# Kernel tuning notes

Measured on AMD Instinct MI355X. Metric: run time of the kernel, lower is better.

Reference implementation:

```python
import jax, jax.numpy as jnp
import numpy as np

B, N, K = 4, 8192, 10
_DIMS = [(12, 64), (64, 64), (128, 64), (64, 64), (128, 64), (192, 1024), (1216, 256), (256, 256), (256, 128), (128, 2)]


def setup_inputs() -> dict:
    key = jax.random.key(0)
    keys = jax.random.split(key, 12)
    inp = {"targets": jax.random.normal(keys[0], (B, N, 3), dtype=jnp.float32)}
    for i, (ci, co) in enumerate(_DIMS):
        a = float(np.sqrt(0.75 / ci))  # init_params: uniform(-sqrt(0.75/fan_in), +)
        inp[f"w{i + 1}"] = jax.random.uniform(keys[i + 1], (ci, co), minval=-a, maxval=a, dtype=jnp.float32)
    inp["prelu_a"] = 0.25 * jnp.ones((10,), jnp.float32)  # nn.PReLU default slope
    return inp


def _prelu(x, a):
    return jnp.where(x >= 0, x, a * x)


def _graph_features(x, k):
    # x: [N, C] -> edge features [N, k, 2C] (knn gather, diff, concat center)
    x2 = jnp.sum(x * x, axis=-1)
    d = x2[:, None] + x2[None, :] - 2.0 * (x @ x.T)  # [N, N] sq dists
    _, idx = jax.lax.top_k(-d, k)  # k nearest (includes self)
    nb = x[idx]  # [N, k, C]
    xr = jnp.broadcast_to(x[:, None, :], nb.shape)
    return jnp.concatenate([nb - xr, xr], axis=-1)


def _edge_conv(x, wa_list, k):
    # x: [B, N, C]; shared-MLP on edge features then max over k neighbors
    f = jax.vmap(lambda xb: _graph_features(xb, k))(x)  # [B, N, k, 2C]
    for w, a in wa_list:
        f = _prelu(f @ w, a)
    return jnp.max(f, axis=-2)  # [B, N, Cout]


def _forward(targets, ws, pa):
    # loss_f(targets) = 0.5*||targets||^2  =>  targets_grad = targets
    g = jax.grad(lambda t: 0.5 * jnp.sum(t * t))(targets)
    x = jnp.concatenate([targets, g], axis=-1)  # [B, N, 6]; hidden_features=0
    x1 = _edge_conv(x, [(ws[0], pa[0]), (ws[1], pa[1])], K)
    x2 = _edge_conv(x1, [(ws[2], pa[2]), (ws[3], pa[3])], K)
    x3 = _edge_conv(x2, [(ws[4], pa[4])], K)
    x4 = jnp.concatenate([x1, x2, x3], axis=-1)  # [B, N, 192]
    x5 = _prelu(x4 @ ws[5], pa[5])  # [B, N, 1024]
    x5 = jnp.broadcast_to(jnp.max(x5, axis=-2, keepdims=True), x5.shape)  # global max, repeated
    y = jnp.concatenate([x1, x2, x3, x5], axis=-1)  # [B, N, 1216]
    for i in range(6, 10):  # dropout is identity at eval
        y = _prelu(y @ ws[i], pa[i])
    return y[..., : 2]  # lr = y[..., :num_losses*2]; hidden slice is empty


def reference(targets, w1, w2, w3, w4, w5, w6, w7, w8, w9, w10, prelu_a):
    ws = [w1, w2, w3, w4, w5, w6, w7, w8, w9, w10]
    return _forward(targets, ws, prelu_a)
```

## Files before the change

kernel.cpp:

```cpp
#include <hip/hip_runtime.h>
#include <math.h>

#define NPTS 8192
#define KNNK 10

typedef __attribute__((ext_vector_type(8))) short bf16x8s;
typedef __attribute__((ext_vector_type(4))) float f32x4;

__device__ __forceinline__ float preluf(float v, float a){ return v >= 0.f ? v : a*v; }
__device__ __forceinline__ float4 f4fma(float a, float4 b, float4 c){
  return make_float4(fmaf(a,b.x,c.x), fmaf(a,b.y,c.y), fmaf(a,b.z,c.z), fmaf(a,b.w,c.w));
}

__device__ __forceinline__ void gl_lds16(const void* g, void* l){
  __builtin_amdgcn_global_load_lds((const __attribute__((address_space(1))) void*)g,
                                   (__attribute__((address_space(3))) void*)l, 16, 0, 0);
}
__device__ __forceinline__ void gl_lds4(const void* g, void* l){
  __builtin_amdgcn_global_load_lds((const __attribute__((address_space(1))) void*)g,
                                   (__attribute__((address_space(3))) void*)l, 4, 0, 0);
}

__device__ __forceinline__ void kinsd2(double* bk, float& g9, float pbd9, float d, int j){
  if (__any(d < g9)) {
    double t = (double)d;
    t = __longlong_as_double(__double_as_longlong(t) | (unsigned long long)(unsigned)j);
    #pragma unroll
    for (int s=0;s<10;++s){
      double mn = fmin(bk[s], t);
      double mx = fmax(bk[s], t);
      bk[s] = mn; t = mx;
    }
    g9 = fminf((float)bk[9], pbd9);
  }
}

__device__ __forceinline__ unsigned bfsplit2(float a, float b, unsigned& lo2){
  unsigned ua = __float_as_uint(a), ub = __float_as_uint(b);
  unsigned ha = (ua + 0x7FFFu + ((ua>>16)&1u)) & 0xFFFF0000u;
  unsigned hb = (ub + 0x7FFFu + ((ub>>16)&1u)) & 0xFFFF0000u;
  float ra = a - __uint_as_float(ha);
  float rb = b - __uint_as_float(hb);
  unsigned la = __float_as_uint(ra), lb = __float_as_uint(rb);
  unsigned qa = (la + 0x7FFFu + ((la>>16)&1u)) >> 16;
  unsigned qb = (lb + 0x7FFFu + ((lb>>16)&1u)) & 0xFFFF0000u;
  lo2 = qa | qb;
  return (ha >> 16) | hb;
}

__global__ __launch_bounds__(256) void prep0_kernel(const float* __restrict__ T,
                                                    float* __restrict__ x0,
                                                    float* __restrict__ sqn){
  int p = blockIdx.x*256 + threadIdx.x;
  float t0 = T[p*3+0], t1 = T[p*3+1], t2 = T[p*3+2];
  *(float4*)(x0 + (size_t)p*4) = make_float4(t0,t1,t2,0.f);
  float s = fmaf(t0,t0,0.f); s = fmaf(t1,t1,s); s = fmaf(t2,t2,s); s = fmaf(0.f,0.f,s);
  sqn[p] = s;
}

__global__ __launch_bounds__(256, 4) void knn64_kernel(const unsigned short* __restrict__ Xh,
                                                       const unsigned short* __restrict__ Xl,
                                                       const float* __restrict__ sqn,
                                                       double* __restrict__ pk){
  __shared__ __align__(16) unsigned char smem[33792];
  float* sx2j = (float*)(smem + 32768);
  double* lst = (double*)smem;

  const int b   = blockIdx.y;
  const int q0  = blockIdx.x * 64;
  const int jh  = blockIdx.z;
  const int tid = threadIdx.x;
  const int L   = tid & 63;
  const int w   = tid >> 6;
  const int lm  = L & 15;
  const int kg  = L >> 4;

  const size_t bbase = (size_t)b * NPTS;
  const int qi = q0 + w*16 + lm;

  bf16x8s qh[2], ql[2];
  {
    const char* Qh = (const char*)Xh + (bbase + qi)*128;
    const char* Ql = (const char*)Xl + (bbase + qi)*128;
    #pragma unroll
    for (int kc=0;kc<2;++kc){
      qh[kc] = *(const bf16x8s*)(Qh + kc*64 + kg*16);
      ql[kc] = *(const bf16x8s*)(Ql + kc*64 + kg*16);
    }
  }
  const float x2q = sqn[bbase + qi];

  const int srow = L >> 3;
  const unsigned soff = (unsigned)(((L & 7) ^ srow) << 4);
  const char* srch = (const char*)Xh + (bbase + (size_t)jh*4096 + w*32 + srow)*128 + soff;
  const char* srcl = (const char*)Xl + (bbase + (size_t)jh*4096 + w*32 + srow)*128 + soff;
  const float* sx2jsrc = sqn + bbase + jh*4096 + w*64 + L;

  #pragma unroll
  for (int i=0;i<4;++i){
    gl_lds16(srch + i*1024, smem + w*4096 + i*1024);
    gl_lds16(srcl + i*1024, smem + 16384 + w*4096 + i*1024);
  }
  if (w < 2) gl_lds4(sx2jsrc, (char*)sx2j + w*256);

  double bk[10];
  float g9 = INFINITY, pbd9 = INFINITY;
  #pragma unroll
  for (int u=0;u<10;++u) bk[u] = (double)INFINITY;

  const char* xjh_c = (const char*)smem;
  const char* xjl_c = (const char*)smem + 16384;
  const unsigned swz = (unsigned)((lm & 7) << 4);

  for (int t = 0; t < 32; ++t) {
    __syncthreads();

    f32x4 acc[8];
    #pragma unroll
    for (int jb=0;jb<8;++jb) acc[jb] = (f32x4){0.f,0.f,0.f,0.f};

    #pragma unroll
    for (int kc=0;kc<2;++kc){
      const unsigned koff = (unsigned)(kc*64 + kg*16) ^ swz;
      #pragma unroll
      for (int jb=0;jb<8;++jb){
        const int rb = (jb*16 + lm)*128;
        bf16x8s jhf = *(const bf16x8s*)(xjh_c + rb + koff);
        bf16x8s jlf = *(const bf16x8s*)(xjl_c + rb + koff);
        acc[jb] = __builtin_amdgcn_mfma_f32_16x16x32_bf16(jhf, qh[kc], acc[jb], 0,0,0);
        acc[jb] = __builtin_amdgcn_mfma_f32_16x16x32_bf16(jlf, qh[kc], acc[jb], 0,0,0);
        acc[jb] = __builtin_amdgcn_mfma_f32_16x16x32_bf16(jhf, ql[kc], acc[jb], 0,0,0);
      }
    }
    __syncthreads();

    if (t < 31){
      const char* nh = srch + (size_t)(t+1)*16384;
      const char* nl = srcl + (size_t)(t+1)*16384;
      #pragma unroll
      for (int i=0;i<4;++i){
        gl_lds16(nh + i*1024, smem + w*4096 + i*1024);
        gl_lds16(nl + i*1024, smem + 16384 + w*4096 + i*1024);
      }
      if (w < 2) gl_lds4(sx2jsrc + (size_t)(t+1)*128, (char*)sx2j + ((t+1)&1)*512 + w*256);
    }

    const int j0 = jh*4096 + t*128;
    const float* x2jb = sx2j + (t&1)*128;

    #pragma unroll
    for (int jb=0;jb<8;++jb){
      float4 xj2 = *(const float4*)&x2jb[jb*16 + kg*4];
      f32x4 c = acc[jb];
      float4 dv = make_float4(x2q + xj2.x - 2.0f*c[0],
                              x2q + xj2.y - 2.0f*c[1],
                              x2q + xj2.z - 2.0f*c[2],
                              x2q + xj2.w - 2.0f*c[3]);
      float m4 = fminf(fminf(dv.x,dv.y), fminf(dv.z,dv.w));
      if (__any(m4 < g9)){
        const int jj = j0 + jb*16 + kg*4;
        kinsd2(bk, g9, pbd9, dv.x, jj);
        kinsd2(bk, g9, pbd9, dv.y, jj+1);
        kinsd2(bk, g9, pbd9, dv.z, jj+2);
        kinsd2(bk, g9, pbd9, dv.w, jj+3);
      }
      if (jb & 1){
        float d9 = (float)bk[9];
        float m  = fminf(d9, __shfl_xor(d9, 16));
        float mm = fminf(m,  __shfl_xor(m, 32));
        pbd9 = mm;
        g9 = mm;
      }
    }
  }

  __syncthreads();
  #pragma unroll
  for (int u=0;u<10;++u) lst[(size_t)(w*16 + lm)*40 + kg*10 + u] = bk[u];
  __syncthreads();
  if (tid < 64) {
    const double* row = &lst[(size_t)tid*40];
    int i0=0, i1=0, i2=0, i3=0;
    size_t base = ((size_t)jh*(4*NPTS) + bbase + q0 + tid)*10;
    #pragma unroll
    for (int u=0;u<10;++u){
      double ka = row[i0], kb2 = row[10+i1], kc2 = row[20+i2], kd2 = row[30+i3];
      bool tab = ka  < kb2; double mab = tab ? ka  : kb2;
      bool tcd = kc2 < kd2; double mcd = tcd ? kc2 : kd2;
      bool tt  = mab < mcd; double m   = tt  ? mab : mcd;
      pk[base+u] = m;
      i0 += (tt && tab)  ? 1 : 0;
      i1 += (tt && !tab) ? 1 : 0;
      i2 += (!tt && tcd) ? 1 : 0;
      i3 += (!tt && !tcd)? 1 : 0;
    }
  }
}

__global__ __launch_bounds__(256, 4) void knn4_kernel(const float* __restrict__ X,
                                                      const float* __restrict__ sqn,
                                                      double* __restrict__ pk){
  __shared__ __align__(16) unsigned char smem[20480];
  double* lst = (double*)smem;

  const int b   = blockIdx.y;
  const int q0  = blockIdx.x * 64;
  const int jh  = blockIdx.z;
  const int tid = threadIdx.x;
  const int L   = tid & 63;
  const int w   = tid >> 6;
  const int lm  = L & 15;
  const int kg  = L >> 4;

  const size_t bbase = (size_t)b * NPTS;
  const int qi = q0 + w*16 + lm;
  const float4 q4 = *(const float4*)(X + (bbase + qi)*4);
  const float x2q = sqn[bbase + qi];

  const char* srcj  = (const char*)(X + (bbase + (size_t)jh*4096)*4);
  const float* srcs = sqn + bbase + jh*4096;

  gl_lds16(srcj + (size_t)(w*64 + L)*16, smem + w*1024);
  gl_lds4 (srcs + w*64 + L, smem + 8192 + w*256);

  double bk[10];
  float g9 = INFINITY, pbd9 = INFINITY;
  #pragma unroll
  for (int u=0;u<10;++u) bk[u] = (double)INFINITY;

  for (int t = 0; t < 16; ++t) {
    __syncthreads();
    if (t < 15){
      const int nb = (t+1)&1;
      gl_lds16(srcj + (size_t)(t+1)*4096 + (size_t)(w*64 + L)*16, smem + nb*4096 + w*1024);
      gl_lds4 (srcs + (t+1)*256 + w*64 + L, smem + 8192 + nb*1024 + w*256);
    }
    const float* xj  = (const float*)(smem + (t&1)*4096);
    const float* x2j = (const float*)(smem + 8192 + (t&1)*1024);
    const int j0 = jh*4096 + t*256;

    #pragma unroll
    for (int jb=0;jb<16;++jb){
      const int r0 = jb*16 + kg*4;
      float d0,d1,d2,d3;
      {
        float4 xv = *(const float4*)&xj[(r0+0)*4];
        float acc = fmaf(q4.x, xv.x, 0.f); acc = fmaf(q4.y, xv.y, acc);
        acc = fmaf(q4.z, xv.z, acc);       acc = fmaf(q4.w, xv.w, acc);
        d0 = x2q + x2j[r0+0] - 2.f*acc;
      }
      {
        float4 xv = *(const float4*)&xj[(r0+1)*4];
        float acc = fmaf(q4.x, xv.x, 0.f); acc = fmaf(q4.y, xv.y, acc);
        acc = fmaf(q4.z, xv.z, acc);       acc = fmaf(q4.w, xv.w, acc);
        d1 = x2q + x2j[r0+1] - 2.f*acc;
      }
      {
        float4 xv = *(const float4*)&xj[(r0+2)*4];
        float acc = fmaf(q4.x, xv.x, 0.f); acc = fmaf(q4.y, xv.y, acc);
        acc = fmaf(q4.z, xv.z, acc);       acc = fmaf(q4.w, xv.w, acc);
        d2 = x2q + x2j[r0+2] - 2.f*acc;
      }
      {
        float4 xv = *(const float4*)&xj[(r0+3)*4];
        float acc = fmaf(q4.x, xv.x, 0.f); acc = fmaf(q4.y, xv.y, acc);
        acc = fmaf(q4.z, xv.z, acc);       acc = fmaf(q4.w, xv.w, acc);
        d3 = x2q + x2j[r0+3] - 2.f*acc;
      }
      float m4 = fminf(fminf(d0,d1), fminf(d2,d3));
      if (__any(m4 < g9)){
        const int jj = j0 + r0;
        kinsd2(bk, g9, pbd9, d0, jj);
        kinsd2(bk, g9, pbd9, d1, jj+1);
        kinsd2(bk, g9, pbd9, d2, jj+2);
        kinsd2(bk, g9, pbd9, d3, jj+3);
      }
      if (jb & 1){
        float d9 = (float)bk[9];
        float m  = fminf(d9, __shfl_xor(d9, 16));
        float mm = fminf(m,  __shfl_xor(m, 32));
        pbd9 = mm;
        g9 = mm;
      }
    }
  }

  __syncthreads();
  #pragma unroll
  for (int u=0;u<10;++u) lst[(size_t)(w*16 + lm)*40 + kg*10 + u] = bk[u];
  __syncthreads();
  if (tid < 64) {
    const double* row = &lst[(size_t)tid*40];
    int i0=0, i1=0, i2=0, i3=0;
    size_t base = ((size_t)jh*(4*NPTS) + bbase + q0 + tid)*10;
    #pragma unroll
    for (int u=0;u<10;++u){
      double ka = row[i0], kb2 = row[10+i1], kc2 = row[20+i2], kd2 = row[30+i3];
      bool tab = ka  < kb2; double mab = tab ? ka  : kb2;
      bool tcd = kc2 < kd2; double mcd = tcd ? kc2 : kd2;
      bool tt  = mab < mcd; double m   = tt  ? mab : mcd;
      pk[base+u] = m;
      i0 += (tt && tab)  ? 1 : 0;
      i1 += (tt && !tab) ? 1 : 0;
      i2 += (!tt && tcd) ? 1 : 0;
      i3 += (!tt && !tcd)? 1 : 0;
    }
  }
}

__global__ __launch_bounds__(256) void knnmerge_kernel(const double* __restrict__ pk,
                                                       int* __restrict__ idxout){
  int p = blockIdx.x*256 + threadIdx.x;
  const double* A = pk + (size_t)p*10;
  const double* B = pk + (size_t)(4*NPTS)*10 + (size_t)p*10;
  int ia=0, ib=0;
  int* op = idxout + (size_t)p*10;
  #pragma unroll
  for (int u=0;u<10;++u){
    double ka = A[ia], kb = B[ib];
    bool t = ka < kb;
    op[u] = (int)(__double_as_longlong(t ? ka : kb) & 8191LL);
    ia += t ? 1 : 0; ib += t ? 0 : 1;
  }
}

__global__ __launch_bounds__(256) void prepUD64_kernel(const float* __restrict__ XC, int cin,
                                                       const float* __restrict__ W,
                                                       float* __restrict__ U,
                                                       float* __restrict__ D){
  const int tid = threadIdx.x;
  const int w = tid >> 6, o = tid & 63;
  const int p = blockIdx.x*4 + w;
  const float* xr = XC + (size_t)p*192 + cin;
  float zu = 0.f, zd = 0.f;
  #pragma unroll
  for (int c=0;c<64;++c){
    float xc = xr[c];
    float wt = W[c*64 + o];
    float wb = W[(64+c)*64 + o];
    zu = fmaf(xc, wt, zu);
    zd = fmaf(xc, wb - wt, zd);
  }
  U[(size_t)p*64 + o] = zu;
  D[(size_t)p*64 + o] = zd;
}

__global__ __launch_bounds__(256) void prepUD12_kernel(const float* __restrict__ T,
                                                       const float* __restrict__ W1,
                                                       float* __restrict__ U,
                                                       float* __restrict__ D){
  int p = blockIdx.x*256 + threadIdx.x;
  float t[3] = {T[p*3+0], T[p*3+1], T[p*3+2]};
  const float4* W = (const float4*)W1;
  float4 u[16], q[16];
  #pragma unroll
  for (int o=0;o<16;++o){ u[o]=make_float4(0,0,0,0); q[o]=make_float4(0,0,0,0); }
  #pragma unroll
  for (int c=0;c<3;++c){
    const float tc = t[c];
    #pragma unroll
    for (int o=0;o<16;++o){
      float4 ws  = W[c*16+o],     ws2 = W[(c+3)*16+o];
      float4 wq  = W[(c+6)*16+o], wq2 = W[(c+9)*16+o];
      u[o] = f4fma(tc, make_float4(ws.x+ws2.x, ws.y+ws2.y, ws.z+ws2.z, ws.w+ws2.w), u[o]);
      q[o] = f4fma(tc, make_float4(wq.x+wq2.x, wq.y+wq2.y, wq.z+wq2.z, wq.w+wq2.w), q[o]);
    }
  }
  float4* up = (float4*)(U + (size_t)p*64);
  float4* dp = (float4*)(D + (size_t)p*64);
  #pragma unroll
  for (int o=0;o<16;++o){
    up[o] = u[o];
    dp[o] = make_float4(q[o].x-u[o].x, q[o].y-u[o].y, q[o].z-u[o].z, q[o].w-u[o].w);
  }
}

__global__ __launch_bounds__(256) void edge2w_kernel(const float* __restrict__ U,
                                                     const float* __restrict__ Dp,
                                                     const int* __restrict__ idx,
                                                     const float* __restrict__ Wb,
                                                     const float* __restrict__ PA, int paa, int pab,
                                                     float* __restrict__ out, int coff,
                                                     float* __restrict__ sqnout,
                                                     unsigned short* __restrict__ Xh,
                                                     unsigned short* __restrict__ Xl){
  __shared__ __align__(16) float sh[4][10][68];
  const int tid = threadIdx.x;
  const int w = tid >> 6, o = tid & 63;
  const int p = blockIdx.x*4 + w, b = p >> 13;
  const float aa = PA[paa], ab = PA[pab];

  float wreg[64];
  #pragma unroll
  for (int c=0;c<64;++c) wreg[c] = Wb[c*64 + o];

  const float dc = Dp[(size_t)p*64 + o];

  #pragma unroll
  for (int k=0;k<10;++k){
    int nb = idx[p*10 + k];
    float u = U[((size_t)(b<<13)+nb)*64 + o];
    sh[w][k][o] = preluf(u + dc, aa);
  }
  __syncthreads();

  float mx = -INFINITY;
  #pragma unroll 2
  for (int k=0;k<10;++k){
    float a0=0.f,a1=0.f,a2=0.f,a3=0.f;
    #pragma unroll
    for (int c4=0;c4<16;++c4){
      float4 hv = *(const float4*)&sh[w][k][c4*4];
      a0 = fmaf(hv.x, wreg[c4*4+0], a0);
      a1 = fmaf(hv.y, wreg[c4*4+1], a1);
      a2 = fmaf(hv.z, wreg[c4*4+2], a2);
      a3 = fmaf(hv.w, wreg[c4*4+3], a3);
    }
    float z = (a0+a1)+(a2+a3);
    mx = fmaxf(mx, preluf(z, ab));
  }
  out[(size_t)p*192 + coff + o] = mx;
  {
    unsigned um = __float_as_uint(mx);
    unsigned h  = (um + 0x7FFFu + ((um>>16)&1u)) & 0xFFFF0000u;
    float rr = mx - __uint_as_float(h);
    unsigned ur = __float_as_uint(rr);
    unsigned l  = (ur + 0x7FFFu + ((ur>>16)&1u)) >> 16;
    Xh[(size_t)p*64 + o] = (unsigned short)(h >> 16);
    Xl[(size_t)p*64 + o] = (unsigned short)l;
  }
  float sq = mx*mx;
  #pragma unroll
  for (int off=1; off<64; off<<=1) sq += __shfl_xor(sq, off);
  if (o == 0) sqnout[p] = sq;
}

__global__ __launch_bounds__(256) void edge1w_kernel(const float* __restrict__ U,
                                                     const float* __restrict__ Dp,
                                                     const int* __restrict__ idx,
                                                     const float* __restrict__ PA, int paa,
                                                     float* __restrict__ out, int coff){
  const int tid = threadIdx.x;
  const int w = tid >> 6, o = tid & 63;
  const int p = blockIdx.x*4 + w, b = p >> 13;
  const float aa = PA[paa];
  const float dc = Dp[(size_t)p*64 + o];
  float mx = -INFINITY;
  #pragma unroll
  for (int k=0;k<10;++k){
    int nb = idx[p*10 + k];
    float u = U[((size_t)(b<<13)+nb)*64 + o];
    mx = fmaxf(mx, preluf(u + dc, aa));
  }
  out[(size_t)p*192 + coff + o] = mx;
}

__global__ __launch_bounds__(256) void prepWall_kernel(const float* __restrict__ W6,
                                                       const float* __restrict__ W7,
                                                       const float* __restrict__ W8,
                                                       const float* __restrict__ W9,
                                                       unsigned short* __restrict__ Wh6, unsigned short* __restrict__ Wl6,
                                                       unsigned short* __restrict__ Wh7, unsigned short* __restrict__ Wl7,
                                                       unsigned short* __restrict__ Wh8, unsigned short* __restrict__ Wl8,
                                                       unsigned short* __restrict__ Wh9, unsigned short* __restrict__ Wl9){
  int bb = blockIdx.x;
  const float* W; unsigned short *Wh, *Wl; int K, N, k;
  if (bb < 192)      { W=W6; Wh=Wh6; Wl=Wl6; K=192; N=1024; k=bb; }
  else if (bb < 384) { W=W7; Wh=Wh7; Wl=Wl7; K=192; N=256;  k=bb-192; }
  else if (bb < 640) { W=W8; Wh=Wh8; Wl=Wl8; K=256; N=256;  k=bb-384; }
  else               { W=W9; Wh=Wh9; Wl=Wl9; K=256; N=128;  k=bb-640; }
  for (int n = threadIdx.x; n < N; n += 256){
    float v = W[(size_t)k*N + n];
    unsigned ua = __float_as_uint(v);
    unsigned h = (ua + 0x7FFFu + ((ua>>16)&1u)) & 0xFFFF0000u;
    float r = v - __uint_as_float(h);
    unsigned ub = __float_as_uint(r);
    unsigned l = (ub + 0x7FFFu + ((ub>>16)&1u)) >> 16;
    Wh[(size_t)n*K + k] = (unsigned short)(h >> 16);
    Wl[(size_t)n*K + k] = (unsigned short)l;
  }
}

template<int EPI>
__global__ __launch_bounds__(256, 2) void mgemm_kernel(const float* __restrict__ A, int lda,
                                                       const unsigned short* __restrict__ WhT,
                                                       const unsigned short* __restrict__ WlT,
                                                       int K,
                                                       float* __restrict__ C, int ldc,
                                                       const float* __restrict__ bias,
                                                       const float* __restrict__ PA, int pidx,
                                                       int Ntot){
  __shared__ __align__(16) unsigned char smem[73728];
  unsigned short* sa = (unsigned short*)smem;
  unsigned short* sb = (unsigned short*)(smem + 36864);
  float* cst = (float*)smem;

  const int tid = threadIdx.x;
  const int m0 = blockIdx.x*128, n0 = blockIdx.y*128;
  const int L = tid & 63, w = tid >> 6;
  const int lm = L & 15, kg = L >> 4;

  f32x4 acc[2][8];
  #pragma unroll
  for (int mt=0;mt<2;++mt)
    #pragma unroll
    for (int nt=0;nt<8;++nt) acc[mt][nt] = (f32x4){0.f,0.f,0.f,0.f};

  for (int c0 = 0; c0 < K; c0 += 64) {
    __syncthreads();
    #pragma unroll
    for (int s=0;s<8;++s){
      int e = tid + s*256;
      int r = e >> 4, kq = (e & 15) << 2;
      float4 v = *(const float4*)(A + (size_t)(m0+r)*lda + c0 + kq);
      unsigned lo01, lo23;
      unsigned hi01 = bfsplit2(v.x, v.y, lo01);
      unsigned hi23 = bfsplit2(v.z, v.w, lo23);
      uint2 hp; hp.x = hi01; hp.y = hi23;
      uint2 lp; lp.x = lo01; lp.y = lo23;
      *(uint2*)&sa[r*72 + kq]        = hp;
      *(uint2*)&sa[9216 + r*72 + kq] = lp;
    }
    #pragma unroll
    for (int s=0;s<4;++s){
      int e = tid + s*256;
      int col = e >> 3, ko = (e & 7) << 3;
      *(uint4*)&sb[col*72 + ko]        = *(const uint4*)&WhT[(size_t)(n0+col)*K + c0 + ko];
      *(uint4*)&sb[9216 + col*72 + ko] = *(const uint4*)&WlT[(size_t)(n0+col)*K + c0 + ko];
    }
    __syncthreads();

    #pragma unroll
    for (int kc=0;kc<2;++kc){
      const int ko = kc*32 + kg*8;
      bf16x8s ah[2], al[2];
      #pragma unroll
      for (int mt=0;mt<2;++mt){
        int q = w*32 + mt*16 + lm;
        ah[mt] = *(const bf16x8s*)&sa[q*72 + ko];
        al[mt] = *(const bf16x8s*)&sa[9216 + q*72 + ko];
      }
      #pragma unroll
      for (int nt=0;nt<8;++nt){
        int n = nt*16 + lm;
        bf16x8s bh = *(const bf16x8s*)&sb[n*72 + ko];
        bf16x8s bl = *(const bf16x8s*)&sb[9216 + n*72 + ko];
        #pragma unroll
        for (int mt=0;mt<2;++mt){
          acc[mt][nt] = __builtin_amdgcn_mfma_f32_16x16x32_bf16(ah[mt], bh, acc[mt][nt], 0,0,0);
          acc[mt][nt] = __builtin_amdgcn_mfma_f32_16x16x32_bf16(ah[mt], bl, acc[mt][nt], 0,0,0);
          acc[mt][nt] = __builtin_amdgcn_mfma_f32_16x16x32_bf16(al[mt], bh, acc[mt][nt], 0,0,0);
        }
      }
    }
  }
  __syncthreads();

  const float a = PA[pidx];
  if (EPI == 2) {
    #pragma unroll
    for (int nt=0;nt<8;++nt){
      f32x4 c0v = acc[0][nt], c1v = acc[1][nt];
      float m = -INFINITY;
      #pragma unroll
      for (int r=0;r<4;++r){ m = fmaxf(m, preluf(c0v[r], a)); m = fmaxf(m, preluf(c1v[r], a)); }
      m = fmaxf(m, __shfl_xor(m, 16));
      m = fmaxf(m, __shfl_xor(m, 32));
      if (kg == 0) cst[w*128 + nt*16 + lm] = m;
    }
    __syncthreads();
    if (tid < 128){
      float m = fmaxf(fmaxf(cst[tid], cst[128+tid]), fmaxf(cst[256+tid], cst[384+tid]));
      C[(size_t)blockIdx.x*Ntot + n0 + tid] = m;
    }
  } else {
    float bc[8];
    if (EPI == 1){
      int bb = m0 >> 13;
      #pragma unroll
      for (int nt=0;nt<8;++nt) bc[nt] = bias[bb*256 + n0 + nt*16 + lm];
    }
    #pragma unroll
    for (int mt=0;mt<2;++mt){
      #pragma unroll
      for (int nt=0;nt<8;++nt){
        f32x4 c = acc[mt][nt];
        int col = nt*16 + lm;
        #pragma unroll
        for (int r=0;r<4;++r){
          int row = w*32 + mt*16 + kg*4 + r;
          float v = c[r] + (EPI==1 ? bc[nt] : 0.f);
          cst[row*132 + col] = preluf(v, a);
        }
      }
    }
    __syncthreads();
    const int tm = tid & 15, tn = tid >> 4;
    #pragma unroll
    for (int i=0;i<8;++i){
      int row = tm*8 + i;
      float4 v0 = *(const float4*)&cst[row*132 + tn*8];
      float4 v1 = *(const float4*)&cst[row*132 + tn*8 + 4];
      float* cp = C + (size_t)(m0 + row)*ldc + n0 + tn*8;
      *(float4*)cp     = v0;
      *(float4*)(cp+4) = v1;
    }
  }
}

__global__ __launch_bounds__(256) void reduce_pmax(const float* __restrict__ pmax,
                                                   float* __restrict__ x5m){
  int t = blockIdx.x*256 + threadIdx.x;
  if (t < 4096) {
    int b = t >> 10, o = t & 1023;
    float m = -INFINITY;
    for (int mt=0; mt<64; ++mt) m = fmaxf(m, pmax[((size_t)(b*64+mt))*1024 + o]);
    x5m[t] = m;
  }
}

__global__ __launch_bounds__(256) void bias7_kernel(const float* __restrict__ x5m,
                                                    const float* __restrict__ W7,
                                                    float* __restrict__ b7){
  int b = blockIdx.x; int o = threadIdx.x;
  float s = 0.f;
  for (int j=0;j<1024;++j) s = fmaf(x5m[b*1024+j], W7[(size_t)(192+j)*256 + o], s);
  b7[b*256+o] = s;
}

__global__ __launch_bounds__(256) void final10_kernel(const float* __restrict__ y3,
                                                      const float* __restrict__ W10,
                                                      const float* __restrict__ PA,
                                                      float* __restrict__ out){
  int p = blockIdx.x*256 + threadIdx.x;
  const float4* r = (const float4*)(y3 + (size_t)p*128);
  float s0=0.f, s1=0.f;
  #pragma unroll
  for (int c4=0;c4<32;++c4){
    float4 v = r[c4];
    s0 = fmaf(v.x, W10[(c4*4+0)*2+0], s0); s1 = fmaf(v.x, W10[(c4*4+0)*2+1], s1);
    s0 = fmaf(v.y, W10[(c4*4+1)*2+0], s0); s1 = fmaf(v.y, W10[(c4*4+1)*2+1], s1);
    s0 = fmaf(v.z, W10[(c4*4+2)*2+0], s0); s1 = fmaf(v.z, W10[(c4*4+2)*2+1], s1);
    s0 = fmaf(v.w, W10[(c4*4+3)*2+0], s0); s1 = fmaf(v.w, W10[(c4*4+3)*2+1], s1);
  }
  float a = PA[9];
  out[p*2+0] = s0>=0.f? s0 : a*s0;
  out[p*2+1] = s1>=0.f? s1 : a*s1;
}

extern "C" void kernel_launch(void* const* d_in, const int* in_sizes, int n_in,
                              void* d_out, int out_size, void* d_ws, size_t ws_size,
                              hipStream_t stream) {
  const float* T   = (const float*)d_in[0];
  const float* W1  = (const float*)d_in[1];
  const float* W2  = (const float*)d_in[2];
  const float* W3  = (const float*)d_in[3];
  const float* W4  = (const float*)d_in[4];
  const float* W5  = (const float*)d_in[5];
  const float* W6  = (const float*)d_in[6];
  const float* W7  = (const float*)d_in[7];
  const float* W8  = (const float*)d_in[8];
  const float* W9  = (const float*)d_in[9];
  const float* W10 = (const float*)d_in[10];
  const float* PA  = (const float*)d_in[11];

  float* ws   = (float*)d_ws;
  float* x0   = ws + 0;
  float* sqn0 = ws + 131072;
  float* sqn1 = ws + 163840;
  float* sqn2 = ws + 196608;
  int*   idx0 = (int*)(ws + 229376);
  int*   idx1 = (int*)(ws + 557056);
  int*   idx2 = (int*)(ws + 884736);
  float* xcat = ws + 1212416;
  float* pmax = ws + 7503872;
  float* x5m  = ws + 7766016;
  float* b7   = ws + 7770112;
  float* y1   = ws + 7771136;
  float* y2   = ws + 16159744;
  float* y3   = xcat;
  float* U    = y1;
  float* D    = y2;
  double* pk  = (double*)y1;
  unsigned short* Xh = (unsigned short*)(y1 + 3145728);
  unsigned short* Xl = (unsigned short*)(y1 + 4194304);

  unsigned short* wsc = (unsigned short*)(ws + 229376);
  unsigned short* Wh6 = wsc;
  unsigned short* Wl6 = wsc + 196608;
  unsigned short* Wh7 = wsc + 393216;
  unsigned short* Wl7 = wsc + 442368;
  unsigned short* Wh8 = wsc + 491520;
  unsigned short* Wl8 = wsc + 557056;
  unsigned short* Wh9 = wsc + 622592;
  unsigned short* Wl9 = wsc + 655360;

  prep0_kernel<<<128, 256, 0, stream>>>(T, x0, sqn0);
  knn4_kernel<<<dim3(128,4,2), 256, 0, stream>>>(x0, sqn0, pk);
  knnmerge_kernel<<<128, 256, 0, stream>>>(pk, idx0);
  prepUD12_kernel<<<128, 256, 0, stream>>>(T, W1, U, D);
  edge2w_kernel<<<8192, 256, 0, stream>>>(U, D, idx0, W2, PA, 0, 1, xcat, 0, sqn1, Xh, Xl);

  knn64_kernel<<<dim3(128,4,2), 256, 0, stream>>>(Xh, Xl, sqn1, pk);
  knnmerge_kernel<<<128, 256, 0, stream>>>(pk, idx1);
  prepUD64_kernel<<<8192, 256, 0, stream>>>(xcat, 0, W3, U, D);
  edge2w_kernel<<<8192, 256, 0, stream>>>(U, D, idx1, W4, PA, 2, 3, xcat, 64, sqn2, Xh, Xl);

  knn64_kernel<<<dim3(128,4,2), 256, 0, stream>>>(Xh, Xl, sqn2, pk);
  knnmerge_kernel<<<128, 256, 0, stream>>>(pk, idx2);
  prepUD64_kernel<<<8192, 256, 0, stream>>>(xcat, 64, W5, U, D);
  edge1w_kernel<<<8192, 256, 0, stream>>>(U, D, idx2, PA, 4, xcat, 128);

  prepWall_kernel<<<896, 256, 0, stream>>>(W6, W7, W8, W9,
                                           Wh6, Wl6, Wh7, Wl7, Wh8, Wl8, Wh9, Wl9);

  mgemm_kernel<2><<<dim3(256,8), 256, 0, stream>>>(xcat, 192, Wh6, Wl6, 192, pmax, 0, nullptr, PA, 5, 1024);
  reduce_pmax<<<16, 256, 0, stream>>>(pmax, x5m);
  bias7_kernel<<<4, 256, 0, stream>>>(x5m, W7, b7);
  mgemm_kernel<1><<<dim3(256,2), 256, 0, stream>>>(xcat, 192, Wh7, Wl7, 192, y1, 256, b7, PA, 6, 0);
  mgemm_kernel<0><<<dim3(256,2), 256, 0, stream>>>(y1, 256, Wh8, Wl8, 256, y2, 256, nullptr, PA, 7, 0);
  mgemm_kernel<0><<<dim3(256,1), 256, 0, stream>>>(y2, 256, Wh9, Wl9, 256, y3, 128, nullptr, PA, 8, 0);
  final10_kernel<<<128, 256, 0, stream>>>(y3, W10, PA, (float*)d_out);
}
```

Baseline: 1.517 ms.

## Buffer kNN candidates per lane and flush to sorted list in batches

Replaces the per-candidate insertion into the 10-entry sorted top-k list with a 4-slot per-lane candidate buffer. Candidates below the threshold are appended, and the buffer is merged into the sorted list only when some lane fills it. The wave-wide threshold is refreshed after each flush rather than every two column blocks. This targets divergent insertion sweeps where only a few lanes insert, at the cost of a staler pruning threshold, more registers for the buffer doubles, and select overhead on every push.

New measurement: 1.333 ms. 12.1% less time.

```diff
diff --git a/kernel.cpp b/kernel.cpp
--- a/kernel.cpp
+++ b/kernel.cpp
@@ -21,17 +21,38 @@
                                    (__attribute__((address_space(3))) void*)l, 4, 0, 0);
 }
 
-__device__ __forceinline__ void kinsd2(double* bk, float& g9, float pbd9, float d, int j){
-  if (__any(d < g9)) {
-    double t = (double)d;
-    t = __longlong_as_double(__double_as_longlong(t) | (unsigned long long)(unsigned)j);
-    #pragma unroll
-    for (int s=0;s<10;++s){
-      double mn = fmin(bk[s], t);
-      double mx = fmax(bk[s], t);
-      bk[s] = mn; t = mx;
-    }
-    g9 = fminf((float)bk[9], pbd9);
+__device__ __forceinline__ void kins_raw(double* bk, double t){
+  #pragma unroll
+  for (int s=0;s<10;++s){
+    double mn = fmin(bk[s], t);
+    double mx = fmax(bk[s], t);
+    bk[s] = mn; t = mx;
+  }
+}
+
+__device__ __forceinline__ void kpush(double& b0, double& b1, double& b2, double& b3,
+                                      int& cnt, double* bk, float& g9, float d, int j){
+  bool a = d < g9;
+  if (__any(a ? 1 : 0)) {
+    if (a) {
+      double t = __longlong_as_double(__double_as_longlong((double)d) | (unsigned long long)(unsigned)j);
+      b0 = (cnt==0) ? t : b0;
+      b1 = (cnt==1) ? t : b1;
+      b2 = (cnt==2) ? t : b2;
+      b3 = (cnt==3) ? t : b3;
+      ++cnt;
+    }
+    if (__any(cnt >= 4)) {
+      if (__any(cnt > 0)) kins_raw(bk, b0);
+      if (__any(cnt > 1)) kins_raw(bk, b1);
+      if (__any(cnt > 2)) kins_raw(bk, b2);
+      if (__any(cnt > 3)) kins_raw(bk, b3);
+      b0 = b1 = b2 = b3 = (double)INFINITY;
+      cnt = 0;
+      float d9 = (float)bk[9];
+      float m  = fminf(d9, __shfl_xor(d9, 16));
+      g9 = fminf(m, __shfl_xor(m, 32));
+    }
   }
 }
 
@@ -104,7 +125,9 @@
   if (w < 2) gl_lds4(sx2jsrc, (char*)sx2j + w*256);
 
   double bk[10];
-  float g9 = INFINITY, pbd9 = INFINITY;
+  double b0 = (double)INFINITY, b1 = (double)INFINITY, b2 = (double)INFINITY, b3 = (double)INFINITY;
+  int cnt = 0;
+  float g9 = INFINITY;
   #pragma unroll
   for (int u=0;u<10;++u) bk[u] = (double)INFINITY;
 
@@ -159,20 +182,18 @@
       float m4 = fminf(fminf(dv.x,dv.y), fminf(dv.z,dv.w));
       if (__any(m4 < g9)){
         const int jj = j0 + jb*16 + kg*4;
-        kinsd2(bk, g9, pbd9, dv.x, jj);
-        kinsd2(bk, g9, pbd9, dv.y, jj+1);
-        kinsd2(bk, g9, pbd9, dv.z, jj+2);
-        kinsd2(bk, g9, pbd9, dv.w, jj+3);
-      }
-      if (jb & 1){
-        float d9 = (float)bk[9];
-        float m  = fminf(d9, __shfl_xor(d9, 16));
-        float mm = fminf(m,  __shfl_xor(m, 32));
-        pbd9 = mm;
-        g9 = mm;
-      }
-    }
-  }
+        kpush(b0,b1,b2,b3,cnt, bk, g9, dv.x, jj);
+        kpush(b0,b1,b2,b3,cnt, bk, g9, dv.y, jj+1);
+        kpush(b0,b1,b2,b3,cnt, bk, g9, dv.z, jj+2);
+        kpush(b0,b1,b2,b3,cnt, bk, g9, dv.w, jj+3);
+      }
+    }
+  }
+
+  if (__any(cnt > 0)) kins_raw(bk, b0);
+  if (__any(cnt > 1)) kins_raw(bk, b1);
+  if (__any(cnt > 2)) kins_raw(bk, b2);
+  if (__any(cnt > 3)) kins_raw(bk, b3);
 
   __syncthreads();
   #pragma unroll
@@ -224,7 +245,9 @@
   gl_lds4 (srcs + w*64 + L, smem + 8192 + w*256);
 
   double bk[10];
-  float g9 = INFINITY, pbd9 = INFINITY;
+  double b0 = (double)INFINITY, b1 = (double)INFINITY, b2 = (double)INFINITY, b3 = (double)INFINITY;
+  int cnt = 0;
+  float g9 = INFINITY;
   #pragma unroll
   for (int u=0;u<10;++u) bk[u] = (double)INFINITY;
 
@@ -270,20 +293,18 @@
       float m4 = fminf(fminf(d0,d1), fminf(d2,d3));
       if (__any(m4 < g9)){
         const int jj = j0 + r0;
-        kinsd2(bk, g9, pbd9, d0, jj);
-        kinsd2(bk, g9, pbd9, d1, jj+1);
-        kinsd2(bk, g9, pbd9, d2, jj+2);
-        kinsd2(bk, g9, pbd9, d3, jj+3);
-      }
-      if (jb & 1){
-        float d9 = (float)bk[9];
-        float m  = fminf(d9, __shfl_xor(d9, 16));
-        float mm = fminf(m,  __shfl_xor(m, 32));
-        pbd9 = mm;
-        g9 = mm;
-      }
-    }
-  }
+        kpush(b0,b1,b2,b3,cnt, bk, g9, d0, jj);
+        kpush(b0,b1,b2,b3,cnt, bk, g9, d1, jj+1);
+        kpush(b0,b1,b2,b3,cnt, bk, g9, d2, jj+2);
+        kpush(b0,b1,b2,b3,cnt, bk, g9, d3, jj+3);
+      }
+    }
+  }
+
+  if (__any(cnt > 0)) kins_raw(bk, b0);
+  if (__any(cnt > 1)) kins_raw(bk, b1);
+  if (__any(cnt > 2)) kins_raw(bk, b2);
+  if (__any(cnt > 3)) kins_raw(bk, b3);
 
   __syncthreads();
   #pragma unroll
```
